# Kernel tuning notes

Measured on AMD Instinct MI355X. Metric: run time of the kernel, lower is better.

The kernel has to match this reference:

```python
import jax, jax.numpy as jnp
import numpy as np

B, T, HW, N, HID, K, OUT = 8, 64, 64, 64, 64, 2, 1
DT = 0.1


def setup_inputs() -> dict:
    key = jax.random.key(0)
    ks = jax.random.split(key, 16)
    nrm = lambda k, shape, s: jax.random.normal(k, shape, jnp.float32) * s
    return {
        "frames": jax.random.uniform(ks[0], (B, T, HW, HW, 3), jnp.float32),
        "adjacency": jax.random.uniform(ks[1], (B, T, N, N), jnp.float32) / N,
        "hidden0": jnp.zeros((B, N, HID), jnp.float32),
        "Wc1": nrm(ks[2], (32, 3, 3, 3), 0.3), "bc1": jnp.zeros(32, jnp.float32),
        "Wc2": nrm(ks[3], (64, 32, 3, 3), 0.08), "bc2": jnp.zeros(64, jnp.float32),
        "Wc3": nrm(ks[4], (128, 64, 3, 3), 0.06), "bc3": jnp.zeros(128, jnp.float32),
        "We": nrm(ks[5], (128, HID), 0.09), "be": jnp.zeros(HID, jnp.float32),
        "Wh": nrm(ks[6], (K + 1, HID, HID), 0.12),
        "Wx": nrm(ks[7], (K + 1, HID, HID), 0.12),
        "bg": jnp.zeros(HID, jnp.float32),
        "tau": jnp.ones(HID, jnp.float32),
        "Ap": nrm(ks[8], (HID,), 1.0),
        "Wd1": nrm(ks[9], (HID, 128), 0.12), "bd1": jnp.zeros(128, jnp.float32),
        "Wd2": nrm(ks[10], (128, 64), 0.09), "bd2": jnp.zeros(64, jnp.float32),
        "Wd3": nrm(ks[11], (64, OUT), 0.12), "bd3": jnp.zeros(OUT, jnp.float32),
    }


def _conv_relu(x, w, b, stride):
    # torch Conv2d(k=3, stride=2, padding=1) == explicit padding (1,1)
    y = jax.lax.conv_general_dilated(
        x, w, (stride, stride), [(1, 1), (1, 1)],
        dimension_numbers=("NCHW", "OIHW", "NCHW"))
    return jax.nn.relu(y + b[None, :, None, None])


def _forward(frames, adjacency, hidden0, Wc1, bc1, Wc2, bc2, Wc3, bc3,
             We, be, Wh, Wx, bg, tau, Ap, Wd1, bd1, Wd2, bd2, Wd3, bd3):
    Bn, Tn, Hh, Ww, C = frames.shape
    # faithful to torch .view(-1, C, H, W): raw memory reinterpretation
    x = frames.reshape(Bn * Tn, C, Hh, Ww)
    x = _conv_relu(x, Wc1, bc1, 2)   # [BT,32,32,32]
    x = _conv_relu(x, Wc2, bc2, 2)   # [BT,64,16,16]
    x = _conv_relu(x, Wc3, bc3, 2)   # [BT,128,8,8]; AdaptiveAvgPool2d((8,8)) is identity here
    feats = x.reshape(Bn, Tn, 128, 8, 8).transpose(0, 1, 3, 4, 2).reshape(Bn, Tn, 64, 128)
    node = feats @ We + be           # [B,T,N,HID]

    Kp = Wh.shape[0] - 1
    eye = jnp.eye(adjacency.shape[-1], dtype=frames.dtype)

    def step(h, inputs):
        xt, At = inputs              # [B,N,HID], [B,N,N]
        powers = [jnp.broadcast_to(eye, At.shape)]
        p = At
        for _ in range(Kp):          # static K-loop -> [I, A, ..., A^K]
            powers.append(p)
            p = jnp.matmul(p, At)
        S = jnp.stack(powers)        # [K+1,B,N,N]
        z = jnp.einsum("bnd,kde->kbne", h, Wh) + jnp.einsum("bnd,kde->kbne", xt, Wx)
        gc = jnp.einsum("kbnm,kbme->bne", S, z) + bg
        f = jnp.tanh(gc)
        h_next = h + DT * (-(1.0 / tau + f) * h + f * Ap)  # liquid time-constant Euler step
        m = h_next.mean(axis=1)      # [B,HID]
        d = jax.nn.relu(m @ Wd1 + bd1)
        d = jax.nn.relu(d @ Wd2 + bd2)
        c = d @ Wd3 + bd3            # [B,OUT]
        return h_next, c

    xs = (node.transpose(1, 0, 2, 3), adjacency.transpose(1, 0, 2, 3))
    final_h, controls = jax.lax.scan(step, hidden0, xs)
    controls = controls.transpose(1, 0, 2)  # [B,T,OUT]
    return controls, final_h


def reference(frames, adjacency, hidden0, Wc1, bc1, Wc2, bc2, Wc3, bc3,
              We, be, Wh, Wx, bg, tau, Ap, Wd1, bd1, Wd2, bd2, Wd3, bd3):
    return _forward(frames, adjacency, hidden0, Wc1, bc1, Wc2, bc2, Wc3, bc3,
                    We, be, Wh, Wx, bg, tau, Ap, Wd1, bd1, Wd2, bd2, Wd3, bd3)
```

## Files before the change

kernel.cpp:

```cpp
#include <hip/hip_runtime.h>
#include <hip/hip_bf16.h>

#define DT_C 0.1f
#define PS 72

typedef short bfrag __attribute__((ext_vector_type(8)));
typedef _Float16 hfrag __attribute__((ext_vector_type(8)));
typedef float f32x4 __attribute__((ext_vector_type(4)));

union FU { bfrag v; unsigned short s[8]; uint4 q; };
union HU { hfrag v; unsigned short s[8]; uint4 q; };

__device__ __forceinline__ unsigned short bf16_rn(float x) {
  union { float f; unsigned u; } v; v.f = x;
  unsigned r = v.u + 0x7fffu + ((v.u >> 16) & 1u);
  return (unsigned short)(r >> 16);
}
__device__ __forceinline__ float bf16_tof(unsigned short h) {
  union { unsigned u; float f; } v; v.u = ((unsigned)h) << 16; return v.f;
}
__device__ __forceinline__ unsigned short bfu(float x) {
  union { __hip_bfloat16 b; unsigned short u; } cv;
  cv.b = __float2bfloat16(x);
  return cv.u;
}
__device__ __forceinline__ float tanh_f(float x) {
  return 1.0f - 2.0f / (__expf(2.0f * x) + 1.0f);
}
__device__ __forceinline__ void h16split(float v, unsigned short& hu, unsigned short& lu) {
  union { _Float16 h; unsigned short u; } a, b;
  a.h = (_Float16)v;
  b.h = (_Float16)(v - (float)a.h);
  hu = a.u; lu = b.u;
}
__device__ __forceinline__ unsigned short h16hi(float v) {
  union { _Float16 h; unsigned short u; } a; a.h = (_Float16)v; return a.u;
}

__global__ __launch_bounds__(256) void wprep_k(const float* __restrict__ Wc2,
                                               const float* __restrict__ Wc3,
                                               const float* __restrict__ Wh,
                                               const float* __restrict__ We,
                                               const float* __restrict__ Wx,
                                               const float* __restrict__ Wc1,
                                               unsigned short* __restrict__ W2h,
                                               unsigned short* __restrict__ W2l,
                                               unsigned short* __restrict__ W3h,
                                               unsigned short* __restrict__ W3l,
                                               unsigned short* __restrict__ WTh,
                                               unsigned short* __restrict__ WTl,
                                               unsigned short* __restrict__ WeTh,
                                               unsigned short* __restrict__ WeTl,
                                               unsigned short* __restrict__ WxTh,
                                               unsigned short* __restrict__ WxTl,
                                               unsigned short* __restrict__ W1h,
                                               unsigned short* __restrict__ W1l) {
  int i = blockIdx.x * 256 + threadIdx.x;
  if (i < 18432) {
    int oc = i / 288, rem = i % 288, pos = rem >> 5, ic = rem & 31;
    float v = Wc2[oc*288 + ic*9 + pos];
    h16split(v, W2h[i], W2l[i]);
  } else if (i < 92160) {
    int j = i - 18432;
    int oc = j / 576, rem = j % 576, pos = rem >> 6, ic = rem & 63;
    float v = Wc3[oc*576 + ic*9 + pos];
    h16split(v, W3h[j], W3l[j]);
  } else if (i < 104448) {
    int j = i - 92160;
    int k3 = j >> 12, rem = j & 4095, din = rem >> 6, dout = rem & 63;
    float v = Wh[j];
    unsigned short hi = bf16_rn(v);
    WTh[k3*4096 + dout*64 + din] = hi;
    WTl[k3*4096 + dout*64 + din] = bf16_rn(v - bf16_tof(hi));
  } else if (i < 112640) {
    int j = i - 104448;
    int e = j >> 7, oc = j & 127;
    float v = We[oc*64 + e];
    h16split(v, WeTh[j], WeTl[j]);
  } else if (i < 124928) {
    int j = i - 112640;
    int k3 = j >> 12, rem = j & 4095, e = rem >> 6, din = rem & 63;
    float v = Wx[k3*4096 + din*64 + e];
    unsigned short hi = bf16_rn(v);
    WxTh[j] = hi;
    WxTl[j] = bf16_rn(v - bf16_tof(hi));
  } else if (i < 125952) {
    int j = i - 124928;
    int oc = j >> 5, k = j & 31;
    float v = 0.f;
    if (k < 27) { int pos = k / 3, ic = k % 3; v = Wc1[oc*27 + ic*9 + pos]; }
    h16split(v, W1h[j], W1l[j]);
  }
}

#define MFMAH(a, bb, cc) __builtin_amdgcn_mfma_f32_16x16x32_f16((a), (bb), (cc), 0, 0, 0)

__global__ __launch_bounds__(512) void conv1m_k(const float* __restrict__ frames,
                                                const unsigned short* __restrict__ W1h,
                                                const unsigned short* __restrict__ W1l,
                                                const float* __restrict__ bias,
                                                unsigned short* __restrict__ c1h) {
  __shared__ __align__(16) unsigned short sIn[12288];
  int bt = blockIdx.x, tid = threadIdx.x;
  {
    const float4* src = (const float4*)(frames + (size_t)bt * 12288);
    for (int i = tid; i < 3072; i += 512) {
      float4 v = src[i];
      ushort4 h;
      h.x = h16hi(v.x); h.y = h16hi(v.y); h.z = h16hi(v.z); h.w = h16hi(v.w);
      *(ushort4*)&sIn[i*4] = h;
    }
  }
  __syncthreads();
  int lane = tid & 63, w = tid >> 6, g = lane >> 4, c = lane & 15;
  HU Bh[2], Bl[2];
  #pragma unroll
  for (int n = 0; n < 2; ++n) {
    Bh[n].q = *(const uint4*)(W1h + (n*16 + c)*32 + g*8);
    Bl[n].q = *(const uint4*)(W1l + (n*16 + c)*32 + g*8);
  }
  float bv[2] = {bias[c], bias[16 + c]};
  #pragma unroll 1
  for (int im = 0; im < 8; ++im) {
    int mi = w*8 + im;
    int p = mi*16 + c;
    int ho = p >> 5, wo = p & 31;
    HU Af;
    #pragma unroll
    for (int j = 0; j < 8; ++j) {
      int k = 8*g + j;
      unsigned short v = 0;
      if (k < 27) {
        int pos = k / 3, ic = k % 3;
        int hi = 2*ho - 1 + pos/3, wi = 2*wo - 1 + pos%3;
        v = (hi >= 0 && wi >= 0) ? sIn[ic*4096 + hi*64 + wi] : (unsigned short)0;
      }
      Af.s[j] = v;
    }
    f32x4 acc[2] = {{0.f,0.f,0.f,0.f},{0.f,0.f,0.f,0.f}};
    #pragma unroll
    for (int n = 0; n < 2; ++n) {
      acc[n] = MFMAH(Af.v, Bh[n].v, acc[n]);
      acc[n] = MFMAH(Af.v, Bl[n].v, acc[n]);
    }
    #pragma unroll
    for (int n = 0; n < 2; ++n) {
      int oc = n*16 + c;
      int ks3 = oc >> 3, il = oc & 7;
      #pragma unroll
      for (int r = 0; r < 4; ++r) {
        int po = mi*16 + 4*g + r;
        int ho2 = po >> 5, wo2 = po & 31;
        float v = fmaxf(acc[n][r] + bv[n], 0.f);
        size_t dst = (size_t)bt*32768 + ks3*8192
                   + ((size_t)((ho2*2 + (wo2&1))*16 + (wo2>>1)))*8 + il;
        c1h[dst] = h16hi(v);
      }
    }
  }
}

__global__ __launch_bounds__(256) void conv2m_k(const unsigned short* __restrict__ c1h,
                                                const unsigned short* __restrict__ W2h,
                                                const unsigned short* __restrict__ W2l,
                                                const float* __restrict__ bias,
                                                unsigned short* __restrict__ c2h) {
  __shared__ __align__(16) unsigned short sH[32768];
  int bt = blockIdx.x, tid = threadIdx.x;
  {
    const uint4* gh = (const uint4*)(c1h + (size_t)bt*32768);
    for (int i = tid; i < 4096; i += 256) ((uint4*)sH)[i] = gh[i];
  }
  __syncthreads();
  int lane = tid & 63, w = tid >> 6, g = lane >> 4, c = lane & 15;
  f32x4 acc[4][4] = {};
  const uint4 z4 = make_uint4(0,0,0,0);
  #pragma unroll
  for (int pos = 0; pos < 9; ++pos) {
    const int kh = pos / 3, kw = pos % 3;
    HU Ah[4];
    #pragma unroll
    for (int m = 0; m < 4; ++m) {
      int pix = w*64 + m*16 + c;
      int ho = pix >> 4, wo = pix & 15;
      int hi = 2*ho - 1 + kh, wi = 2*wo - 1 + kw;
      bool ok = (hi >= 0) & (wi >= 0);
      int hic = ok ? hi : 0, wic = ok ? wi : 0;
      int a = (((g*32 + hic)*2 + (wic & 1))*16 + (wic >> 1))*8;
      uint4 vh = *(const uint4*)&sH[a];
      Ah[m].q = ok ? vh : z4;
    }
    HU Bh[4], Bl[4];
    #pragma unroll
    for (int n = 0; n < 4; ++n) {
      int off = (n*16 + c)*288 + pos*32 + g*8;
      Bh[n].q = *(const uint4*)(W2h + off);
      Bl[n].q = *(const uint4*)(W2l + off);
    }
    #pragma unroll
    for (int m = 0; m < 4; ++m)
      #pragma unroll
      for (int n = 0; n < 4; ++n) {
        acc[m][n] = MFMAH(Ah[m].v, Bh[n].v, acc[m][n]);
        acc[m][n] = MFMAH(Ah[m].v, Bl[n].v, acc[m][n]);
      }
  }
  #pragma unroll
  for (int n = 0; n < 4; ++n) {
    int oc = n*16 + c;
    float bv = bias[oc];
    int ks3 = oc >> 3, il = oc & 7;
    #pragma unroll
    for (int m = 0; m < 4; ++m) {
      #pragma unroll
      for (int r = 0; r < 4; ++r) {
        int pix = w*64 + m*16 + 4*g + r;
        int ho = pix >> 4, wo = pix & 15;
        float v = fmaxf(acc[m][n][r] + bv, 0.f);
        size_t dst = (size_t)bt*16384 + ((((ks3*16 + ho)*2 + (wo&1))*8 + (wo>>1)))*8 + il;
        c2h[dst] = h16hi(v);
      }
    }
  }
}

__global__ __launch_bounds__(256) void conv3e_k(const unsigned short* __restrict__ c2h,
                                                const unsigned short* __restrict__ W3h,
                                                const unsigned short* __restrict__ W3l,
                                                const float* __restrict__ bias,
                                                const unsigned short* __restrict__ WeTh,
                                                const unsigned short* __restrict__ WeTl,
                                                const float* __restrict__ be,
                                                float* __restrict__ node) {
  __shared__ __align__(16) unsigned short sH[16384];
  __shared__ __align__(16) unsigned short sF[64*136];
  int bt = blockIdx.x, tid = threadIdx.x;
  {
    const uint4* gh = (const uint4*)(c2h + (size_t)bt*16384);
    for (int i = tid; i < 2048; i += 256) ((uint4*)sH)[i] = gh[i];
  }
  __syncthreads();
  int lane = tid & 63, w = tid >> 6, g = lane >> 4, c = lane & 15;
  f32x4 acc[8] = {};
  const uint4 z4 = make_uint4(0,0,0,0);
  int pix = w*16 + c;
  int ho = pix >> 3, wo = pix & 7;
  #pragma unroll
  for (int pos = 0; pos < 9; ++pos) {
    const int kh = pos / 3, kw = pos % 3;
    int hi = 2*ho - 1 + kh, wi = 2*wo - 1 + kw;
    bool ok = (hi >= 0) & (wi >= 0);
    int hic = ok ? hi : 0, wic = ok ? wi : 0;
    #pragma unroll
    for (int ih = 0; ih < 2; ++ih) {
      int icg = ih*4 + g;
      int a = ((((icg*16 + hic)*2 + (wic & 1))*8 + (wic >> 1)))*8;
      HU Ah;
      uint4 vh = *(const uint4*)&sH[a];
      Ah.q = ok ? vh : z4;
      #pragma unroll
      for (int n = 0; n < 8; ++n) {
        int off = (n*16 + c)*576 + pos*64 + ih*32 + g*8;
        HU Bh, Bl;
        Bh.q = *(const uint4*)(W3h + off);
        Bl.q = *(const uint4*)(W3l + off);
        acc[n] = MFMAH(Ah.v, Bh.v, acc[n]);
        acc[n] = MFMAH(Ah.v, Bl.v, acc[n]);
      }
    }
  }
  #pragma unroll
  for (int n = 0; n < 8; ++n) {
    int oc = n*16 + c;
    float bv = bias[oc];
    #pragma unroll
    for (int r = 0; r < 4; ++r) {
      int po = w*16 + 4*g + r;
      sF[po*136 + oc] = h16hi(fmaxf(acc[n][r] + bv, 0.f));
    }
  }
  __syncthreads();
  f32x4 eacc[4] = {{0.f,0.f,0.f,0.f},{0.f,0.f,0.f,0.f},{0.f,0.f,0.f,0.f},{0.f,0.f,0.f,0.f}};
  #pragma unroll
  for (int kt = 0; kt < 4; ++kt) {
    HU Af;
    Af.q = *(const uint4*)&sF[(w*16 + c)*136 + kt*32 + g*8];
    #pragma unroll
    for (int n = 0; n < 4; ++n) {
      int off = (n*16 + c)*128 + kt*32 + g*8;
      HU Bh, Bl;
      Bh.q = *(const uint4*)(WeTh + off);
      Bl.q = *(const uint4*)(WeTl + off);
      eacc[n] = MFMAH(Af.v, Bh.v, eacc[n]);
      eacc[n] = MFMAH(Af.v, Bl.v, eacc[n]);
    }
  }
  #pragma unroll
  for (int n = 0; n < 4; ++n) {
    int e = n*16 + c;
    float bev = be[e];
    #pragma unroll
    for (int r = 0; r < 4; ++r) {
      int po = w*16 + 4*g + r;
      node[(size_t)bt*4096 + po*64 + e] = eacc[n][r] + bev;
    }
  }
}

#define MFMA(a, bb, cc) __builtin_amdgcn_mfma_f32_16x16x32_bf16((a), (bb), (cc), 0, 0, 0)

__global__ __launch_bounds__(512) void prepm_k(const float* __restrict__ adj,
                                               const float* __restrict__ node,
                                               const unsigned short* __restrict__ WxTh,
                                               const unsigned short* __restrict__ WxTl,
                                               unsigned short* __restrict__ Abf,
                                               unsigned short* __restrict__ A2bf,
                                               float* __restrict__ gxg) {
  __shared__ __align__(16) unsigned short sAh[64*PS], sAl[64*PS];
  __shared__ __align__(16) unsigned short sXh[64*PS], sXl[64*PS];
  __shared__ __align__(16) unsigned short sNh[64*PS], sNl[64*PS];
  __shared__ __align__(16) unsigned short sZh[64*PS], sZl[64*PS];
  int bt = blockIdx.x, tid = threadIdx.x;
  int lane = tid & 63, w = tid >> 6, g = lane >> 4, c = lane & 15;
  int mt = w & 3, nt0 = (w >> 2) * 2;
  int mrow = mt*16 + 4*g;
  for (int i = tid; i < 1024; i += 512) {
    int r = i >> 4, c0 = (i & 15) * 4;
    float4 av = ((const float4*)(adj + (size_t)bt*4096))[i];
    float4 nv = ((const float4*)(node + (size_t)bt*4096))[i];
    float aa[4] = {av.x, av.y, av.z, av.w};
    float nn[4] = {nv.x, nv.y, nv.z, nv.w};
    ushort4 ah4, al4, nh4, nl4;
    #pragma unroll
    for (int j = 0; j < 4; ++j) {
      unsigned short hi = bf16_rn(aa[j]);
      unsigned short lo = bf16_rn(aa[j] - bf16_tof(hi));
      ((unsigned short*)&ah4)[j] = hi;
      ((unsigned short*)&al4)[j] = lo;
      sXh[(c0+j)*PS + r] = hi;
      sXl[(c0+j)*PS + r] = lo;
      unsigned short nhi = bf16_rn(nn[j]);
      ((unsigned short*)&nh4)[j] = nhi;
      ((unsigned short*)&nl4)[j] = bf16_rn(nn[j] - bf16_tof(nhi));
    }
    *(ushort4*)&sAh[r*PS + c0] = ah4;
    *(ushort4*)&sAl[r*PS + c0] = al4;
    *(ushort4*)&sNh[r*PS + c0] = nh4;
    *(ushort4*)&sNl[r*PS + c0] = nl4;
    *(ushort4*)&Abf[(size_t)bt*4096 + r*64 + c0] = ah4;
  }
  __syncthreads();
  FU a_h[2], a_l[2], n_h[2], n_l[2];
  #pragma unroll
  for (int kt = 0; kt < 2; ++kt) {
    int ao = (mt*16 + c)*PS + kt*32 + 8*g;
    a_h[kt].q = *(const uint4*)&sAh[ao];
    a_l[kt].q = *(const uint4*)&sAl[ao];
    n_h[kt].q = *(const uint4*)&sNh[ao];
    n_l[kt].q = *(const uint4*)&sNl[ao];
  }
  f32x4 a2f[2] = {{0.f,0.f,0.f,0.f},{0.f,0.f,0.f,0.f}};
  f32x4 zf[2]  = {{0.f,0.f,0.f,0.f},{0.f,0.f,0.f,0.f}};
  #pragma unroll
  for (int tt = 0; tt < 2; ++tt) {
    int e = (nt0+tt)*16 + c;
    #pragma unroll
    for (int kt = 0; kt < 2; ++kt) {
      FU bh, bl;
      int bo = e*PS + kt*32 + 8*g;
      bh.q = *(const uint4*)&sXh[bo];
      bl.q = *(const uint4*)&sXl[bo];
      a2f[tt] = MFMA(a_h[kt].v, bh.v, a2f[tt]);
      a2f[tt] = MFMA(a_l[kt].v, bh.v, a2f[tt]);
      a2f[tt] = MFMA(a_h[kt].v, bl.v, a2f[tt]);
      FU wh, wl;
      int wo = 4096 + e*64 + kt*32 + 8*g;
      wh.q = *(const uint4*)(WxTh + wo);
      wl.q = *(const uint4*)(WxTl + wo);
      zf[tt] = MFMA(n_h[kt].v, wh.v, zf[tt]);
      zf[tt] = MFMA(n_l[kt].v, wh.v, zf[tt]);
      zf[tt] = MFMA(n_h[kt].v, wl.v, zf[tt]);
    }
  }
  __syncthreads();
  #pragma unroll
  for (int tt = 0; tt < 2; ++tt) {
    int e = (nt0+tt)*16 + c;
    ushort4 zh4, zl4;
    #pragma unroll
    for (int r = 0; r < 4; ++r) {
      float va = a2f[tt][r];
      unsigned short ahi = bf16_rn(va);
      sXh[(mrow+r)*PS + e] = ahi;
      sXl[(mrow+r)*PS + e] = bf16_rn(va - bf16_tof(ahi));
      A2bf[(size_t)bt*4096 + (mrow+r)*64 + e] = ahi;
      float vz = zf[tt][r];
      unsigned short zhi = bf16_rn(vz);
      ((unsigned short*)&zh4)[r] = zhi;
      ((unsigned short*)&zl4)[r] = bf16_rn(vz - bf16_tof(zhi));
    }
    *(ushort4*)&sZh[e*PS + mrow] = zh4;
    *(ushort4*)&sZl[e*PS + mrow] = zl4;
  }
  __syncthreads();
  f32x4 gacc[2] = {{0.f,0.f,0.f,0.f},{0.f,0.f,0.f,0.f}};
  #pragma unroll
  for (int tt = 0; tt < 2; ++tt) {
    int e = (nt0+tt)*16 + c;
    zf[tt][0] = 0.f; zf[tt][1] = 0.f; zf[tt][2] = 0.f; zf[tt][3] = 0.f;
    #pragma unroll
    for (int kt = 0; kt < 2; ++kt) {
      FU bh, bl;
      int bo = e*PS + kt*32 + 8*g;
      bh.q = *(const uint4*)&sZh[bo];
      bl.q = *(const uint4*)&sZl[bo];
      gacc[tt] = MFMA(a_h[kt].v, bh.v, gacc[tt]);
      gacc[tt] = MFMA(a_l[kt].v, bh.v, gacc[tt]);
      gacc[tt] = MFMA(a_h[kt].v, bl.v, gacc[tt]);
      FU wh, wl;
      int w0 = e*64 + kt*32 + 8*g;
      wh.q = *(const uint4*)(WxTh + w0);
      wl.q = *(const uint4*)(WxTl + w0);
      gacc[tt] = MFMA(n_h[kt].v, wh.v, gacc[tt]);
      gacc[tt] = MFMA(n_l[kt].v, wh.v, gacc[tt]);
      gacc[tt] = MFMA(n_h[kt].v, wl.v, gacc[tt]);
      int w2 = 8192 + e*64 + kt*32 + 8*g;
      wh.q = *(const uint4*)(WxTh + w2);
      wl.q = *(const uint4*)(WxTl + w2);
      zf[tt] = MFMA(n_h[kt].v, wh.v, zf[tt]);
      zf[tt] = MFMA(n_l[kt].v, wh.v, zf[tt]);
      zf[tt] = MFMA(n_h[kt].v, wl.v, zf[tt]);
    }
  }
  __syncthreads();
  #pragma unroll
  for (int tt = 0; tt < 2; ++tt) {
    int e = (nt0+tt)*16 + c;
    ushort4 zh4, zl4;
    #pragma unroll
    for (int r = 0; r < 4; ++r) {
      float vz = zf[tt][r];
      unsigned short zhi = bf16_rn(vz);
      ((unsigned short*)&zh4)[r] = zhi;
      ((unsigned short*)&zl4)[r] = bf16_rn(vz - bf16_tof(zhi));
    }
    *(ushort4*)&sZh[e*PS + mrow] = zh4;
    *(ushort4*)&sZl[e*PS + mrow] = zl4;
  }
  __syncthreads();
  FU p_h[2], p_l[2];
  #pragma unroll
  for (int kt = 0; kt < 2; ++kt) {
    int po = (mt*16 + c)*PS + kt*32 + 8*g;
    p_h[kt].q = *(const uint4*)&sXh[po];
    p_l[kt].q = *(const uint4*)&sXl[po];
  }
  #pragma unroll
  for (int tt = 0; tt < 2; ++tt) {
    int e = (nt0+tt)*16 + c;
    #pragma unroll
    for (int kt = 0; kt < 2; ++kt) {
      FU bh, bl;
      int bo = e*PS + kt*32 + 8*g;
      bh.q = *(const uint4*)&sZh[bo];
      bl.q = *(const uint4*)&sZl[bo];
      gacc[tt] = MFMA(p_h[kt].v, bh.v, gacc[tt]);
      gacc[tt] = MFMA(p_l[kt].v, bh.v, gacc[tt]);
      gacc[tt] = MFMA(p_h[kt].v, bl.v, gacc[tt]);
    }
    *(float4*)(gxg + (size_t)bt*4096 + e*64 + mrow) =
        make_float4(gacc[tt][0], gacc[tt][1], gacc[tt][2], gacc[tt][3]);
  }
}

__global__ __launch_bounds__(1024, 4) void seq2_k(
    const unsigned short* __restrict__ Abf, const unsigned short* __restrict__ A2bf,
    const float* __restrict__ gxg, const float* __restrict__ h0,
    const unsigned short* __restrict__ WTh, const unsigned short* __restrict__ WTl,
    const float* __restrict__ bg, const float* __restrict__ tau, const float* __restrict__ Apv,
    float* __restrict__ mout, float* __restrict__ out) {
  __shared__ unsigned short sHh[64*72];
  __shared__ unsigned short sA[2][64*72], sA2[2][64*72];
  __shared__ unsigned short sZ1[64*72], sZ2[64*72];
  __shared__ float sPart[64*17];
  int b = blockIdx.x, tid = threadIdx.x;
  int lane = tid & 63, w = tid >> 6, g = lane >> 4, c = lane & 15;
  int mt = w & 3, nt = w >> 2;
  int e = nt*16 + c;
  int mrow = mt*16 + 4*g;
  float itau = 1.f/tau[e], apv = Apv[e], bgv = bg[e];
  FU wf[3][2][2];
  #pragma unroll
  for (int k3 = 0; k3 < 3; ++k3)
    #pragma unroll
    for (int kt = 0; kt < 2; ++kt) {
      int off = k3*4096 + e*64 + kt*32 + 8*g;
      wf[k3][kt][0].q = *(const uint4*)(WTh + off);
      wf[k3][kt][1].q = *(const uint4*)(WTl + off);
    }
  float hm[4];
  #pragma unroll
  for (int r = 0; r < 4; ++r) hm[r] = h0[(size_t)b*4096 + (mrow+r)*64 + e];
  #pragma unroll
  for (int r = 0; r < 4; ++r) sHh[(mrow+r)*72 + e] = bfu(hm[r]);
  {
    int row = tid >> 4, k0 = (tid & 15) * 4;
    *(uint2*)&sA[0][row*72 + k0]  = *(const uint2*)(Abf  + (size_t)b*64*4096 + tid*4);
    *(uint2*)&sA2[0][row*72 + k0] = *(const uint2*)(A2bf + (size_t)b*64*4096 + tid*4);
  }
  __syncthreads();
  #pragma unroll 1
  for (int t = 0; t < 64; ++t) {
    int cur = t & 1;
    size_t bt = (size_t)b*64 + t;
    int tn = (t < 63) ? t + 1 : t;
    uint2 pa  = *(const uint2*)(Abf  + ((size_t)b*64 + tn)*4096 + tid*4);
    uint2 pa2 = *(const uint2*)(A2bf + ((size_t)b*64 + tn)*4096 + tid*4);
    float4 gxv = *(const float4*)(gxg + bt*4096 + e*64 + mrow);
    FU ha[2];
    #pragma unroll
    for (int kt = 0; kt < 2; ++kt)
      ha[kt].q = *(const uint4*)&sHh[(mt*16 + c)*72 + kt*32 + 8*g];
    f32x4 a1 = {0.f,0.f,0.f,0.f}, a2 = {0.f,0.f,0.f,0.f};
    #pragma unroll
    for (int kt = 0; kt < 2; ++kt) {
      a1 = MFMA(ha[kt].v, wf[1][kt][0].v, a1);
      a1 = MFMA(ha[kt].v, wf[1][kt][1].v, a1);
      a2 = MFMA(ha[kt].v, wf[2][kt][0].v, a2);
      a2 = MFMA(ha[kt].v, wf[2][kt][1].v, a2);
    }
    {
      ushort4 o1, o2;
      o1.x = bfu(a1[0]); o1.y = bfu(a1[1]); o1.z = bfu(a1[2]); o1.w = bfu(a1[3]);
      o2.x = bfu(a2[0]); o2.y = bfu(a2[1]); o2.z = bfu(a2[2]); o2.w = bfu(a2[3]);
      *(ushort4*)&sZ1[e*72 + mrow] = o1;
      *(ushort4*)&sZ2[e*72 + mrow] = o2;
    }
    __syncthreads();
    f32x4 acc = {0.f,0.f,0.f,0.f};
    #pragma unroll
    for (int kt = 0; kt < 2; ++kt) {
      FU aA, aA2, z1f, z2f;
      int ao = (mt*16 + c)*72 + kt*32 + 8*g;
      aA.q  = *(const uint4*)&sA[cur][ao];
      aA2.q = *(const uint4*)&sA2[cur][ao];
      z1f.q = *(const uint4*)&sZ1[e*72 + kt*32 + 8*g];
      z2f.q = *(const uint4*)&sZ2[e*72 + kt*32 + 8*g];
      acc = MFMA(ha[kt].v, wf[0][kt][0].v, acc);
      acc = MFMA(ha[kt].v, wf[0][kt][1].v, acc);
      acc = MFMA(aA.v,  z1f.v, acc);
      acc = MFMA(aA2.v, z2f.v, acc);
    }
    float gxa[4] = {gxv.x, gxv.y, gxv.z, gxv.w};
    float ps = 0.f;
    #pragma unroll
    for (int r = 0; r < 4; ++r) {
      float gc = acc[r] + gxa[r] + bgv;
      float f = tanh_f(gc);
      float hn = hm[r] + DT_C * (-(itau + f) * hm[r] + f * apv);
      hm[r] = hn;
      ps += hn;
      sHh[(mrow+r)*72 + e] = bfu(hn);
    }
    sPart[e*17 + mt*4 + g] = ps;
    {
      int row = tid >> 4, k0 = (tid & 15) * 4;
      *(uint2*)&sA[cur^1][row*72 + k0]  = pa;
      *(uint2*)&sA2[cur^1][row*72 + k0] = pa2;
    }
    __syncthreads();
    if (lane < 4) {
      int ee = w*4 + lane;
      float s = 0.f;
      #pragma unroll
      for (int j = 0; j < 16; ++j) s += sPart[ee*17 + j];
      mout[bt*64 + ee] = s * (1.0f / 64.0f);
    }
  }
  #pragma unroll
  for (int r = 0; r < 4; ++r)
    out[512 + (size_t)b*4096 + (mrow+r)*64 + e] = hm[r];
}

__global__ __launch_bounds__(128) void dec_k(const float* __restrict__ mout,
                                             const float* __restrict__ Wd1, const float* __restrict__ bd1,
                                             const float* __restrict__ Wd2, const float* __restrict__ bd2,
                                             const float* __restrict__ Wd3, const float* __restrict__ bd3,
                                             float* __restrict__ out) {
  __shared__ float sm[64], sd1[128], sd2[64];
  int bt = blockIdx.x, tid = threadIdx.x;
  if (tid < 64) sm[tid] = mout[(size_t)bt*64 + tid];
  __syncthreads();
  {
    float a = bd1[tid];
    #pragma unroll 8
    for (int e = 0; e < 64; ++e) a += sm[e] * Wd1[e*128 + tid];
    sd1[tid] = fmaxf(a, 0.f);
  }
  __syncthreads();
  if (tid < 64) {
    float a = bd2[tid];
    #pragma unroll 8
    for (int i = 0; i < 128; ++i) a += sd1[i] * Wd2[i*64 + tid];
    sd2[tid] = fmaxf(a, 0.f);
  }
  __syncthreads();
  if (tid < 64) {
    float p = sd2[tid] * Wd3[tid];
    #pragma unroll
    for (int off = 32; off > 0; off >>= 1) p += __shfl_down(p, off, 64);
    if (tid == 0) out[bt] = p + bd3[0];
  }
}

extern "C" void kernel_launch(void* const* d_in, const int* in_sizes, int n_in,
                              void* d_out, int out_size, void* d_ws, size_t ws_size,
                              hipStream_t stream) {
  const float* frames = (const float*)d_in[0];
  const float* adj    = (const float*)d_in[1];
  const float* h0     = (const float*)d_in[2];
  const float* Wc1 = (const float*)d_in[3];  const float* bc1 = (const float*)d_in[4];
  const float* Wc2 = (const float*)d_in[5];  const float* bc2 = (const float*)d_in[6];
  const float* Wc3 = (const float*)d_in[7];  const float* bc3 = (const float*)d_in[8];
  const float* We  = (const float*)d_in[9];  const float* be  = (const float*)d_in[10];
  const float* Wh  = (const float*)d_in[11]; const float* Wx  = (const float*)d_in[12];
  const float* bg  = (const float*)d_in[13]; const float* tau = (const float*)d_in[14];
  const float* Ap  = (const float*)d_in[15];
  const float* Wd1 = (const float*)d_in[16]; const float* bd1 = (const float*)d_in[17];
  const float* Wd2 = (const float*)d_in[18]; const float* bd2 = (const float*)d_in[19];
  const float* Wd3 = (const float*)d_in[20]; const float* bd3 = (const float*)d_in[21];

  float* ws = (float*)d_ws;
  unsigned short* c1h = (unsigned short*)(ws);
  unsigned short* c2h = (unsigned short*)(ws + 16777216);
  unsigned short* W2h = (unsigned short*)(ws + 20971520);
  unsigned short* W2l = (unsigned short*)(ws + 20980736);
  unsigned short* W3h = (unsigned short*)(ws + 20989952);
  unsigned short* W3l = (unsigned short*)(ws + 21026816);
  unsigned short* WTh = (unsigned short*)(ws + 21063680);
  unsigned short* WTl = (unsigned short*)(ws + 21069824);
  unsigned short* WeTh = (unsigned short*)(ws + 21075968);
  unsigned short* WeTl = (unsigned short*)(ws + 21080064);
  unsigned short* WxTh = (unsigned short*)(ws + 21084160);
  unsigned short* WxTl = (unsigned short*)(ws + 21090304);
  unsigned short* W1h  = (unsigned short*)(ws + 21096448);
  unsigned short* W1l  = (unsigned short*)(ws + 21096960);
  float* node = ws + 4194304;
  float* gx   = ws + 6291456;
  unsigned short* Abf  = (unsigned short*)(ws + 8388608);
  unsigned short* A2bf = (unsigned short*)(ws + 9437184);
  float* mo   = ws + 10485760;
  float* out  = (float*)d_out;

  wprep_k <<<492, 256, 0, stream>>>(Wc2, Wc3, Wh, We, Wx, Wc1, W2h, W2l, W3h, W3l,
                                    WTh, WTl, WeTh, WeTl, WxTh, WxTl, W1h, W1l);
  conv1m_k<<<512, 512, 0, stream>>>(frames, W1h, W1l, bc1, c1h);
  conv2m_k<<<512, 256, 0, stream>>>(c1h, W2h, W2l, bc2, c2h);
  conv3e_k<<<512, 256, 0, stream>>>(c2h, W3h, W3l, bc3, WeTh, WeTl, be, node);
  prepm_k <<<512, 512, 0, stream>>>(adj, node, WxTh, WxTl, Abf, A2bf, gx);
  seq2_k  <<<8,  1024, 0, stream>>>(Abf, A2bf, gx, h0, WTh, WTl, bg, tau, Ap, mo, out);
  dec_k   <<<512, 128, 0, stream>>>(mo, Wd1, bd1, Wd2, bd2, Wd3, bd3, out);
}
```

Before: 263.5 us.

## Fuse conv1 and conv2 into one kernel keeping conv1 output in LDS

Merges the first two convolution kernels so conv1's output tile is written to shared memory and consumed directly by conv2, instead of round-tripping through a global workspace buffer. This removes one kernel launch and the global write and read of the conv1 activations. With 512 threads per block, conv2's work is split across 8 waves, each handling 2 pixel tiles instead of 4. The combined LDS footprint (about 88 KB per block) limits how many blocks can be resident per CU.

```diff
diff --git a/kernel.cpp b/kernel.cpp
--- a/kernel.cpp
+++ b/kernel.cpp
@@ -95,12 +95,16 @@
 
 #define MFMAH(a, bb, cc) __builtin_amdgcn_mfma_f32_16x16x32_f16((a), (bb), (cc), 0, 0, 0)
 
-__global__ __launch_bounds__(512) void conv1m_k(const float* __restrict__ frames,
-                                                const unsigned short* __restrict__ W1h,
-                                                const unsigned short* __restrict__ W1l,
-                                                const float* __restrict__ bias,
-                                                unsigned short* __restrict__ c1h) {
+__global__ __launch_bounds__(512) void c12_k(const float* __restrict__ frames,
+                                             const unsigned short* __restrict__ W1h,
+                                             const unsigned short* __restrict__ W1l,
+                                             const float* __restrict__ bc1,
+                                             const unsigned short* __restrict__ W2h,
+                                             const unsigned short* __restrict__ W2l,
+                                             const float* __restrict__ bc2,
+                                             unsigned short* __restrict__ c2h) {
   __shared__ __align__(16) unsigned short sIn[12288];
+  __shared__ __align__(16) unsigned short sC1[32768];
   int bt = blockIdx.x, tid = threadIdx.x;
   {
     const float4* src = (const float4*)(frames + (size_t)bt * 12288);
@@ -113,81 +117,67 @@
   }
   __syncthreads();
   int lane = tid & 63, w = tid >> 6, g = lane >> 4, c = lane & 15;
-  HU Bh[2], Bl[2];
-  #pragma unroll
-  for (int n = 0; n < 2; ++n) {
-    Bh[n].q = *(const uint4*)(W1h + (n*16 + c)*32 + g*8);
-    Bl[n].q = *(const uint4*)(W1l + (n*16 + c)*32 + g*8);
-  }
-  float bv[2] = {bias[c], bias[16 + c]};
-  #pragma unroll 1
-  for (int im = 0; im < 8; ++im) {
-    int mi = w*8 + im;
-    int p = mi*16 + c;
-    int ho = p >> 5, wo = p & 31;
-    HU Af;
-    #pragma unroll
-    for (int j = 0; j < 8; ++j) {
-      int k = 8*g + j;
-      unsigned short v = 0;
-      if (k < 27) {
-        int pos = k / 3, ic = k % 3;
-        int hi = 2*ho - 1 + pos/3, wi = 2*wo - 1 + pos%3;
-        v = (hi >= 0 && wi >= 0) ? sIn[ic*4096 + hi*64 + wi] : (unsigned short)0;
+  const uint4 z4 = make_uint4(0,0,0,0);
+  {
+    HU Bh[2], Bl[2];
+    #pragma unroll
+    for (int n = 0; n < 2; ++n) {
+      Bh[n].q = *(const uint4*)(W1h + (n*16 + c)*32 + g*8);
+      Bl[n].q = *(const uint4*)(W1l + (n*16 + c)*32 + g*8);
+    }
+    float bv[2] = {bc1[c], bc1[16 + c]};
+    #pragma unroll 1
+    for (int im = 0; im < 8; ++im) {
+      int mi = w*8 + im;
+      int p = mi*16 + c;
+      int ho = p >> 5, wo = p & 31;
+      HU Af;
+      #pragma unroll
+      for (int j = 0; j < 8; ++j) {
+        int k = 8*g + j;
+        unsigned short v = 0;
+        if (k < 27) {
+          int pos = k / 3, ic = k % 3;
+          int hi = 2*ho - 1 + pos/3, wi = 2*wo - 1 + pos%3;
+          v = (hi >= 0 && wi >= 0) ? sIn[ic*4096 + hi*64 + wi] : (unsigned short)0;
+        }
+        Af.s[j] = v;
       }
-      Af.s[j] = v;
-    }
-    f32x4 acc[2] = {{0.f,0.f,0.f,0.f},{0.f,0.f,0.f,0.f}};
-    #pragma unroll
-    for (int n = 0; n < 2; ++n) {
-      acc[n] = MFMAH(Af.v, Bh[n].v, acc[n]);
-      acc[n] = MFMAH(Af.v, Bl[n].v, acc[n]);
-    }
-    #pragma unroll
-    for (int n = 0; n < 2; ++n) {
-      int oc = n*16 + c;
-      int ks3 = oc >> 3, il = oc & 7;
+      f32x4 acc[2] = {{0.f,0.f,0.f,0.f},{0.f,0.f,0.f,0.f}};
       #pragma unroll
-      for (int r = 0; r < 4; ++r) {
-        int po = mi*16 + 4*g + r;
-        int ho2 = po >> 5, wo2 = po & 31;
-        float v = fmaxf(acc[n][r] + bv[n], 0.f);
-        size_t dst = (size_t)bt*32768 + ks3*8192
-                   + ((size_t)((ho2*2 + (wo2&1))*16 + (wo2>>1)))*8 + il;
-        c1h[dst] = h16hi(v);
+      for (int n = 0; n < 2; ++n) {
+        acc[n] = MFMAH(Af.v, Bh[n].v, acc[n]);
+        acc[n] = MFMAH(Af.v, Bl[n].v, acc[n]);
       }
-    }
-  }
-}
-
-__global__ __launch_bounds__(256) void conv2m_k(const unsigned short* __restrict__ c1h,
-                                                const unsigned short* __restrict__ W2h,
-                                                const unsigned short* __restrict__ W2l,
-                                                const float* __restrict__ bias,
-                                                unsigned short* __restrict__ c2h) {
-  __shared__ __align__(16) unsigned short sH[32768];
-  int bt = blockIdx.x, tid = threadIdx.x;
-  {
-    const uint4* gh = (const uint4*)(c1h + (size_t)bt*32768);
-    for (int i = tid; i < 4096; i += 256) ((uint4*)sH)[i] = gh[i];
-  }
-  __syncthreads();
-  int lane = tid & 63, w = tid >> 6, g = lane >> 4, c = lane & 15;
-  f32x4 acc[4][4] = {};
-  const uint4 z4 = make_uint4(0,0,0,0);
+      #pragma unroll
+      for (int n = 0; n < 2; ++n) {
+        int oc = n*16 + c;
+        int ks3 = oc >> 3, il = oc & 7;
+        #pragma unroll
+        for (int r = 0; r < 4; ++r) {
+          int po = mi*16 + 4*g + r;
+          int ho2 = po >> 5, wo2 = po & 31;
+          float v = fmaxf(acc[n][r] + bv[n], 0.f);
+          sC1[ks3*8192 + ((ho2*2 + (wo2&1))*16 + (wo2>>1))*8 + il] = h16hi(v);
+        }
+      }
+    }
+  }
+  __syncthreads();
+  f32x4 acc2[2][4] = {};
   #pragma unroll
   for (int pos = 0; pos < 9; ++pos) {
     const int kh = pos / 3, kw = pos % 3;
-    HU Ah[4];
-    #pragma unroll
-    for (int m = 0; m < 4; ++m) {
-      int pix = w*64 + m*16 + c;
+    HU Ah[2];
+    #pragma unroll
+    for (int m = 0; m < 2; ++m) {
+      int pix = w*32 + m*16 + c;
       int ho = pix >> 4, wo = pix & 15;
       int hi = 2*ho - 1 + kh, wi = 2*wo - 1 + kw;
       bool ok = (hi >= 0) & (wi >= 0);
       int hic = ok ? hi : 0, wic = ok ? wi : 0;
       int a = (((g*32 + hic)*2 + (wic & 1))*16 + (wic >> 1))*8;
-      uint4 vh = *(const uint4*)&sH[a];
+      uint4 vh = *(const uint4*)&sC1[a];
       Ah[m].q = ok ? vh : z4;
     }
     HU Bh[4], Bl[4];
@@ -198,25 +188,25 @@
       Bl[n].q = *(const uint4*)(W2l + off);
     }
     #pragma unroll
-    for (int m = 0; m < 4; ++m)
+    for (int m = 0; m < 2; ++m)
       #pragma unroll
       for (int n = 0; n < 4; ++n) {
-        acc[m][n] = MFMAH(Ah[m].v, Bh[n].v, acc[m][n]);
-        acc[m][n] = MFMAH(Ah[m].v, Bl[n].v, acc[m][n]);
+        acc2[m][n] = MFMAH(Ah[m].v, Bh[n].v, acc2[m][n]);
+        acc2[m][n] = MFMAH(Ah[m].v, Bl[n].v, acc2[m][n]);
       }
   }
   #pragma unroll
   for (int n = 0; n < 4; ++n) {
     int oc = n*16 + c;
-    float bv = bias[oc];
+    float bv = bc2[oc];
     int ks3 = oc >> 3, il = oc & 7;
     #pragma unroll
-    for (int m = 0; m < 4; ++m) {
+    for (int m = 0; m < 2; ++m) {
       #pragma unroll
       for (int r = 0; r < 4; ++r) {
-        int pix = w*64 + m*16 + 4*g + r;
+        int pix = w*32 + m*16 + 4*g + r;
         int ho = pix >> 4, wo = pix & 15;
-        float v = fmaxf(acc[m][n][r] + bv, 0.f);
+        float v = fmaxf(acc2[m][n][r] + bv, 0.f);
         size_t dst = (size_t)bt*16384 + ((((ks3*16 + ho)*2 + (wo&1))*8 + (wo>>1)))*8 + il;
         c2h[dst] = h16hi(v);
       }
@@ -631,7 +621,6 @@
   const float* Wd3 = (const float*)d_in[20]; const float* bd3 = (const float*)d_in[21];
 
   float* ws = (float*)d_ws;
-  unsigned short* c1h = (unsigned short*)(ws);
   unsigned short* c2h = (unsigned short*)(ws + 16777216);
   unsigned short* W2h = (unsigned short*)(ws + 20971520);
   unsigned short* W2l = (unsigned short*)(ws + 20980736);
@@ -654,8 +643,7 @@
 
   wprep_k <<<492, 256, 0, stream>>>(Wc2, Wc3, Wh, We, Wx, Wc1, W2h, W2l, W3h, W3l,
                                     WTh, WTl, WeTh, WeTl, WxTh, WxTl, W1h, W1l);
-  conv1m_k<<<512, 512, 0, stream>>>(frames, W1h, W1l, bc1, c1h);
-  conv2m_k<<<512, 256, 0, stream>>>(c1h, W2h, W2l, bc2, c2h);
+  c12_k   <<<512, 512, 0, stream>>>(frames, W1h, W1l, bc1, W2h, W2l, bc2, c2h);
   conv3e_k<<<512, 256, 0, stream>>>(c2h, W3h, W3l, bc3, WeTh, WeTl, be, node);
   prepm_k <<<512, 512, 0, stream>>>(adj, node, WxTh, WxTl, Abf, A2bf, gx);
   seq2_k  <<<8,  1024, 0, stream>>>(Abf, A2bf, gx, h0, WTh, WTl, bg, tau, Ap, mo, out);
```

Result: no change. 263.5 us (median of 2 runs) (+0.0%).
